# Optimization experiments

Hardware: AMD Instinct MI355X
Metric: run time of the kernel (lower is better)

Reference implementation:

```python
import jax, jax.numpy as jnp
import numpy as np
from jax import lax

COEF = 0.97  # rnn.weight_hh_l0; weight_ih_l0 == 1.0


def setup_inputs() -> dict:
    key = jax.random.key(0)
    B, C, T = 128, 1, 262144
    x = jax.random.normal(key, (B, C, T), dtype=jnp.float32)
    return {"input": x}


def reference(input) -> jnp.ndarray:
    # torch.nn.RNN(1,1,1,bias=False) with weight_ih=1, weight_hh=COEF and
    # default nonlinearity='tanh':  h[t] = tanh(x[t] + COEF * h[t-1])
    x = input[:, 0, :]                     # [B, T]
    B = x.shape[0]

    def step(h, x_t):                      # h: [B], x_t: [B]
        h = jnp.tanh(x_t + COEF * h)
        return h, h

    h0 = jnp.zeros((B,), dtype=x.dtype)
    _, ys = lax.scan(step, h0, x.T)        # ys: [T, B]
    return ys.T[:, None, :]                # [B, 1, T]
```

## Files before the change

### kernel.cpp

```cpp
#include <hip/hip_runtime.h>


#define BB 128
#define TT 262144
#define LL 256
#define WW 64
#define KK 32
#define SPANS 64
#define RR ((WW + LL) / KK)
#define WR (WW / KK)

__global__ __launch_bounds__(64) void ipe_kernel(const float* __restrict__ x,
                                                 float* __restrict__ y) {
    const int lane = threadIdx.x;
    const int blocksPerRow = (TT / LL) / SPANS;
    const int row = blockIdx.x / blocksPerRow;
    const int q   = blockIdx.x % blocksPerRow;
    const size_t rowBase = (size_t)row * TT;

    __shared__ float tile[2][KK][SPANS + 1];

    const int ls = lane & 7;
    const int le = lane >> 3;

    float4 pf[8];

    const long loadBase = (long)(q * SPANS + ls) * LL - WW + 4 * le;

    auto issue_loads = [&](int r) {
        #pragma unroll
        for (int m = 0; m < 8; ++m) {
            const long t = loadBase + (long)m * 8 * LL + (long)r * KK;
            if (t >= 0) {
                pf[m] = *reinterpret_cast<const float4*>(x + rowBase + t);
            } else {
                pf[m] = make_float4(0.f, 0.f, 0.f, 0.f);
            }
        }
    };
    auto write_lds = [&](int b) {
        #pragma unroll
        for (int m = 0; m < 8; ++m) {
            float* p = &tile[b][4 * le][8 * m + ls];
            p[0 * (SPANS + 1)] = pf[m].x;
            p[1 * (SPANS + 1)] = pf[m].y;
            p[2 * (SPANS + 1)] = pf[m].z;
            p[3 * (SPANS + 1)] = pf[m].w;
        }
    };

    issue_loads(0);
    write_lds(0);
    issue_loads(1);
    __syncthreads();

    const float C2 = 2.885390081777926815f;
    const float K2 = 0.97f * C2;
    float h = 0.f;

    for (int r = 0; r < RR; ++r) {
        const int b = r & 1;
        if (r >= WR) {
            #pragma unroll
            for (int k = 0; k < KK; ++k) {
                float xs = tile[b][k][lane] * C2;
                float z2 = fmaf(K2, h, xs);
                float ez = __builtin_amdgcn_exp2f(z2);
                float rc = __builtin_amdgcn_rcpf(ez + 1.0f);
                h = fmaf(-2.0f, rc, 1.0f);
                tile[b][k][lane] = h;
            }
        } else {
            #pragma unroll
            for (int k = 0; k < KK; ++k) {
                float xs = tile[b][k][lane] * C2;
                float z2 = fmaf(K2, h, xs);
                float ez = __builtin_amdgcn_exp2f(z2);
                float rc = __builtin_amdgcn_rcpf(ez + 1.0f);
                h = fmaf(-2.0f, rc, 1.0f);
            }
        }
        __syncthreads();

        if (r >= WR) {
            #pragma unroll
            for (int m = 0; m < 8; ++m) {
                const int s = 8 * m + ls;
                const long t = (long)(q * SPANS + s) * LL + (long)r * KK - WW + 4 * le;
                const float* p = &tile[b][4 * le][s];
                float4 v;
                v.x = p[0 * (SPANS + 1)];
                v.y = p[1 * (SPANS + 1)];
                v.z = p[2 * (SPANS + 1)];
                v.w = p[3 * (SPANS + 1)];
                *reinterpret_cast<float4*>(y + rowBase + t) = v;
            }
        }
        if (r + 1 < RR) {
            write_lds(b ^ 1);
            if (r + 2 < RR) issue_loads(r + 2);
        }
        __syncthreads();
    }
}

extern "C" void kernel_launch(void* const* d_in, const int* in_sizes, int n_in,
                              void* d_out, int out_size, void* d_ws, size_t ws_size,
                              hipStream_t stream) {
    const float* x = (const float*)d_in[0];
    float* y = (float*)d_out;
    const int grid = BB * (TT / LL) / SPANS;
    ipe_kernel<<<dim3(grid), dim3(64), 0, stream>>>(x, y);
}
```

Baseline: 52.82 us.

## Pack four independent waves per block with private LDS tiles and drop barriers

Each 256-thread block now holds four waves, and each wave works on its own 64-span group with a private LDS tile, so the __syncthreads barriers go away. Inputs pass through LDS as float4 rows and are read back into a register array before the serial tanh recurrence, and outputs are written back the same way, which replaces scalar transposed LDS access with vector access. Prefetching uses two register buffers that alternate between rounds. The risks are higher register pressure from the two buffers plus the 32-element array, and relying on wave-level ordering with only compiler barriers for correctness of the LDS traffic.

```diff
diff --git a/kernel.cpp b/kernel.cpp
--- a/kernel.cpp
+++ b/kernel.cpp
@@ -6,101 +6,93 @@
 #define LL 256
 #define WW 64
 #define KK 32
-#define SPANS 64
 #define RR ((WW + LL) / KK)
 #define WR (WW / KK)
 
-__global__ __launch_bounds__(64) void ipe_kernel(const float* __restrict__ x,
-                                                 float* __restrict__ y) {
-    const int lane = threadIdx.x;
-    const int blocksPerRow = (TT / LL) / SPANS;
-    const int row = blockIdx.x / blocksPerRow;
-    const int q   = blockIdx.x % blocksPerRow;
+__global__ __launch_bounds__(256) void ipe_kernel(const float* __restrict__ x,
+                                                  float* __restrict__ y) {
+    const int tid  = threadIdx.x;
+    const int lane = tid & 63;
+    const int wv   = tid >> 6;
+    const int w    = blockIdx.x * 4 + wv;
+    const int row  = w >> 4;
+    const int qg   = w & 15;
+    const int s0   = qg * 64;
     const size_t rowBase = (size_t)row * TT;
 
-    __shared__ float tile[2][KK][SPANS + 1];
+    __shared__ float tile_all[4][64][36];
+    float (*tile)[36] = tile_all[wv];
 
     const int ls = lane & 7;
     const int le = lane >> 3;
+    const long loadBase = (long)(s0 + ls) * LL - WW + 4 * le;
 
-    float4 pf[8];
+    float4 pfA[8], pfB[8];
 
-    const long loadBase = (long)(q * SPANS + ls) * LL - WW + 4 * le;
-
-    auto issue_loads = [&](int r) {
+    auto issue = [&](float4 (&pf)[8], int r) {
         #pragma unroll
         for (int m = 0; m < 8; ++m) {
             const long t = loadBase + (long)m * 8 * LL + (long)r * KK;
-            if (t >= 0) {
-                pf[m] = *reinterpret_cast<const float4*>(x + rowBase + t);
-            } else {
-                pf[m] = make_float4(0.f, 0.f, 0.f, 0.f);
-            }
+            if (t >= 0) pf[m] = *reinterpret_cast<const float4*>(x + rowBase + t);
+            else        pf[m] = make_float4(0.f, 0.f, 0.f, 0.f);
         }
     };
-    auto write_lds = [&](int b) {
-        #pragma unroll
-        for (int m = 0; m < 8; ++m) {
-            float* p = &tile[b][4 * le][8 * m + ls];
-            p[0 * (SPANS + 1)] = pf[m].x;
-            p[1 * (SPANS + 1)] = pf[m].y;
-            p[2 * (SPANS + 1)] = pf[m].z;
-            p[3 * (SPANS + 1)] = pf[m].w;
-        }
-    };
-
-    issue_loads(0);
-    write_lds(0);
-    issue_loads(1);
-    __syncthreads();
 
     const float C2 = 2.885390081777926815f;
     const float K2 = 0.97f * C2;
     float h = 0.f;
 
-    for (int r = 0; r < RR; ++r) {
-        const int b = r & 1;
-        if (r >= WR) {
-            #pragma unroll
-            for (int k = 0; k < KK; ++k) {
-                float xs = tile[b][k][lane] * C2;
-                float z2 = fmaf(K2, h, xs);
-                float ez = __builtin_amdgcn_exp2f(z2);
-                float rc = __builtin_amdgcn_rcpf(ez + 1.0f);
-                h = fmaf(-2.0f, rc, 1.0f);
-                tile[b][k][lane] = h;
-            }
-        } else {
-            #pragma unroll
-            for (int k = 0; k < KK; ++k) {
-                float xs = tile[b][k][lane] * C2;
-                float z2 = fmaf(K2, h, xs);
-                float ez = __builtin_amdgcn_exp2f(z2);
-                float rc = __builtin_amdgcn_rcpf(ez + 1.0f);
-                h = fmaf(-2.0f, rc, 1.0f);
-            }
+    issue(pfA, 0);
+
+    auto round = [&](float4 (&cur)[8], float4 (&nxt)[8], int r) {
+        if (r + 1 < RR) issue(nxt, r + 1);
+
+        #pragma unroll
+        for (int m = 0; m < 8; ++m)
+            *reinterpret_cast<float4*>(&tile[8 * m + ls][4 * le]) = cur[m];
+        asm volatile("" ::: "memory");
+
+        float xv[KK];
+        #pragma unroll
+        for (int e = 0; e < 8; ++e) {
+            float4 v = *reinterpret_cast<const float4*>(&tile[lane][4 * e]);
+            xv[4 * e + 0] = v.x; xv[4 * e + 1] = v.y;
+            xv[4 * e + 2] = v.z; xv[4 * e + 3] = v.w;
         }
-        __syncthreads();
+
+        #pragma unroll
+        for (int k = 0; k < KK; ++k) {
+            float z2 = fmaf(K2, h, xv[k] * C2);
+            float ez = __builtin_amdgcn_exp2f(z2);
+            float rc = __builtin_amdgcn_rcpf(ez + 1.0f);
+            h = fmaf(-2.0f, rc, 1.0f);
+            xv[k] = h;
+        }
 
         if (r >= WR) {
+            asm volatile("" ::: "memory");
+            #pragma unroll
+            for (int e = 0; e < 8; ++e) {
+                float4 v;
+                v.x = xv[4 * e + 0]; v.y = xv[4 * e + 1];
+                v.z = xv[4 * e + 2]; v.w = xv[4 * e + 3];
+                *reinterpret_cast<float4*>(&tile[lane][4 * e]) = v;
+            }
+            asm volatile("" ::: "memory");
             #pragma unroll
             for (int m = 0; m < 8; ++m) {
-                const int s = 8 * m + ls;
-                const long t = (long)(q * SPANS + s) * LL + (long)r * KK - WW + 4 * le;
-                const float* p = &tile[b][4 * le][s];
-                float4 v;
-                v.x = p[0 * (SPANS + 1)];
-                v.y = p[1 * (SPANS + 1)];
-                v.z = p[2 * (SPANS + 1)];
-                v.w = p[3 * (SPANS + 1)];
+                float4 v = *reinterpret_cast<const float4*>(&tile[8 * m + ls][4 * le]);
+                const long t = loadBase + (long)m * 8 * LL + (long)r * KK;
                 *reinterpret_cast<float4*>(y + rowBase + t) = v;
             }
         }
-        if (r + 1 < RR) {
-            write_lds(b ^ 1);
-            if (r + 2 < RR) issue_loads(r + 2);
-        }
-        __syncthreads();
+        asm volatile("" ::: "memory");
+    };
+
+    #pragma unroll 1
+    for (int r = 0; r < RR; r += 2) {
+        round(pfA, pfB, r);
+        round(pfB, pfA, r + 1);
     }
 }
 
@@ -109,6 +101,6 @@
                               hipStream_t stream) {
     const float* x = (const float*)d_in[0];
     float* y = (float*)d_out;
-    const int grid = BB * (TT / LL) / SPANS;
-    ipe_kernel<<<dim3(grid), dim3(64), 0, stream>>>(x, y);
+    const int blocks = (BB * (TT / LL)) / (4 * 64);
+    ipe_kernel<<<dim3(blocks), dim3(256), 0, stream>>>(x, y);
 }
```

Result: faster. 51.39 us (-2.7%).
